# Kernel optimization log

Measured on AMD Instinct MI355X. Metric: run time of the kernel, lower is better.

Reference implementation:

```python
import jax, jax.numpy as jnp
import numpy as np

# dims: T time steps, B batch, CIN/COUT conv channels, HxW spatial, K kernel
T, B, CIN, COUT, H, Wd, K = 10, 32, 3, 64, 64, 64, 3
DECAY = 0.2      # LIF leak factor
INH = 1.625      # lateral inhibition strength (mode='threshold')


def setup_inputs() -> dict:
    key = jax.random.key(0)
    k1, k2 = jax.random.split(key)
    x = (jax.random.uniform(k1, (T, B, CIN, H, Wd)) < 0.2).astype(jnp.float32)
    W = jax.random.normal(k2, (COUT, CIN, K, K), dtype=jnp.float32)
    # normweight(): zero-mean, unit-std (biased) per output filter
    W = W - W.mean(axis=(1, 2, 3), keepdims=True)
    W = W / W.reshape(COUT, -1).std(axis=1).reshape(COUT, 1, 1, 1)
    return {"x": x, "W": W}


def _conv(x, W):
    # Conv2d stride=1, padding=1, no bias, NCHW/OIHW
    return jax.lax.conv_general_dilated(
        x, W, window_strides=(1, 1), padding=((1, 1), (1, 1)),
        dimension_numbers=("NCHW", "OIHW", "NCHW"))


def reference(x, W):
    def step(mem, x_t):
        i = _conv(x_t, W)                                        # (B,COUT,H,W)
        # ATB: adaptive per-channel threshold = max over batch+spatial
        thr = jnp.max(i, axis=(0, 2, 3), keepdims=True) + 1e-4   # (1,COUT,1,1)
        # ASF: clamp then thresholded sigmoid filter
        cur = jnp.maximum(i, 0.0)
        i_asf = thr * jax.nn.sigmoid((cur - 0.4 * thr) * (8.0 / thr))
        # LIF update with threshold = thr (set by ATB)
        mem = mem * DECAY + i_asf
        s = (mem > thr).astype(mem.dtype)                        # spikes 0/1
        # WTA k=1: keep only the strongest spiking channel per location
        score = mem * s
        winner = jnp.argmax(score, axis=1)                       # (B,H,W)
        oh = jnp.moveaxis(jax.nn.one_hot(winner, COUT, dtype=mem.dtype), -1, 1)
        s = s * oh
        # membrane reset of fired neurons
        mem = mem * (1.0 - s)
        # lateral inhibition: suppress non-winners at spiking locations
        any_sp = jnp.max(s, axis=1, keepdims=True)
        mem = mem - INH * thr * any_sp * (1.0 - s)
        return mem, s

    mem0 = jnp.zeros((B, COUT, H, Wd), jnp.float32)
    _, spikes = jax.lax.scan(step, mem0, x)
    return spikes  # (T,B,COUT,H,W)
```

## Files before the change

kernel.cpp:

```cpp
#include <hip/hip_runtime.h>
#include <math.h>

#define TT 10
#define BB 32
#define CIN 3
#define COUT 64
#define HH 64
#define WW 64
#define HW (HH*WW)
#define DECAY 0.2f
#define INH 1.625f

__device__ __forceinline__ unsigned int enc_f(float f) {
    unsigned int u = __float_as_uint(f);
    return (u & 0x80000000u) ? ~u : (u | 0x80000000u);
}
__device__ __forceinline__ float dec_f(unsigned int u) {
    u = (u & 0x80000000u) ? (u & 0x7FFFFFFFu) : ~u;
    return __uint_as_float(u);
}

__global__ __launch_bounds__(256) void thr_kernel(
    const float* __restrict__ x,
    const float* __restrict__ Wt,
    unsigned int* __restrict__ thr_raw,
    float* __restrict__ out)
{
    __shared__ float sx[CIN][6][68];
    __shared__ float wmax[4][COUT];

    const int tid  = threadIdx.x;
    const int lane = tid & 63;
    const int wave = tid >> 6;
    const int h0   = blockIdx.x * 4;
    const int b    = blockIdx.y;
    const int t    = blockIdx.z;

    float w[27];
    #pragma unroll
    for (int k = 0; k < 27; k++) w[k] = Wt[lane * 27 + k];

    const float* xb = x + ((size_t)t * BB + b) * (CIN * HW);
    for (int l = tid; l < CIN * 6 * 66; l += 256) {
        int ci  = l / 396;
        int r   = (l % 396) / 66;
        int col = l % 66;
        int gh = h0 + r - 1;
        int gw = col - 1;
        float v = 0.f;
        if (gh >= 0 && gh < HH && gw >= 0 && gw < WW)
            v = xb[ci * HW + gh * WW + gw];
        sx[ci][r][col] = v;
    }
    __syncthreads();

    float* ob = out + (((size_t)t * BB + b) * COUT) * HW;
    float mx = -INFINITY;

    for (int cc = 0; cc < 8; cc++) {
        #pragma unroll
        for (int k = 0; k < 2; k++) {
            int l   = (cc * 2 + k) * 256 + tid;
            int row = l >> 4;
            int q   = l & 15;
            int c   = row >> 2;
            int hr  = row & 3;
            *(float4*)(ob + (size_t)c * HW + (h0 + hr) * WW + q * 4) =
                make_float4(0.f, 0.f, 0.f, 0.f);
        }

        float acc[8];
        #pragma unroll
        for (int j = 0; j < 8; j++) acc[j] = 0.f;

        #pragma unroll
        for (int ci = 0; ci < CIN; ci++)
            #pragma unroll
            for (int kh = 0; kh < 3; kh++) {
                const float* rp = &sx[ci][wave + kh][cc * 8];
                float4 qa = *(const float4*)(rp + 0);
                float4 qb = *(const float4*)(rp + 4);
                float2 qc = *(const float2*)(rp + 8);
                float f0 = qa.x, f1 = qa.y, f2 = qa.z, f3 = qa.w;
                float f4 = qb.x, f5 = qb.y, f6 = qb.z, f7 = qb.w;
                float f8 = qc.x, f9 = qc.y;
                const float w0 = w[ci * 9 + kh * 3 + 0];
                const float w1 = w[ci * 9 + kh * 3 + 1];
                const float w2 = w[ci * 9 + kh * 3 + 2];
                acc[0] = fmaf(w0, f0, acc[0]); acc[0] = fmaf(w1, f1, acc[0]); acc[0] = fmaf(w2, f2, acc[0]);
                acc[1] = fmaf(w0, f1, acc[1]); acc[1] = fmaf(w1, f2, acc[1]); acc[1] = fmaf(w2, f3, acc[1]);
                acc[2] = fmaf(w0, f2, acc[2]); acc[2] = fmaf(w1, f3, acc[2]); acc[2] = fmaf(w2, f4, acc[2]);
                acc[3] = fmaf(w0, f3, acc[3]); acc[3] = fmaf(w1, f4, acc[3]); acc[3] = fmaf(w2, f5, acc[3]);
                acc[4] = fmaf(w0, f4, acc[4]); acc[4] = fmaf(w1, f5, acc[4]); acc[4] = fmaf(w2, f6, acc[4]);
                acc[5] = fmaf(w0, f5, acc[5]); acc[5] = fmaf(w1, f6, acc[5]); acc[5] = fmaf(w2, f7, acc[5]);
                acc[6] = fmaf(w0, f6, acc[6]); acc[6] = fmaf(w1, f7, acc[6]); acc[6] = fmaf(w2, f8, acc[6]);
                acc[7] = fmaf(w0, f7, acc[7]); acc[7] = fmaf(w1, f8, acc[7]); acc[7] = fmaf(w2, f9, acc[7]);
            }

        #pragma unroll
        for (int j = 0; j < 8; j++) mx = fmaxf(mx, acc[j]);
    }

    wmax[wave][lane] = mx;
    __syncthreads();
    if (wave == 0) {
        float m = fmaxf(fmaxf(wmax[0][lane], wmax[1][lane]),
                        fmaxf(wmax[2][lane], wmax[3][lane]));
        atomicMax(&thr_raw[t * COUT + lane], enc_f(m));
    }
}

__global__ __launch_bounds__(256) void fused_kernel(
    const float* __restrict__ x,
    const float* __restrict__ Wt,
    const unsigned int* __restrict__ thr_raw,
    float* __restrict__ out)
{
    __shared__ float sx[TT][CIN][3][36];

    const int tid  = threadIdx.x;
    const int lane = tid & 63;
    const int wave = tid >> 6;
    const int p0   = __builtin_amdgcn_readfirstlane(wave * 8);
    const int b    = blockIdx.x >> 7;
    const int h    = (blockIdx.x >> 1) & 63;
    const int w0   = (blockIdx.x & 1) << 5;

    float w[27];
    #pragma unroll
    for (int k = 0; k < 27; k++) w[k] = Wt[lane * 27 + k];

    {
        const float* xb0 = x + (size_t)b * (CIN * HW);
        for (int l = tid; l < TT * 306; l += 256) {
            int t   = l / 306;
            int r0  = l - t * 306;
            int ci  = r0 / 102;
            int r1  = r0 - ci * 102;
            int r   = r1 / 34;
            int col = r1 - r * 34;
            int gh = h + r - 1;
            int gw = w0 + col - 1;
            float v = 0.f;
            if (gh >= 0 && gh < HH && gw >= 0 && gw < WW)
                v = xb0[(size_t)t * ((size_t)BB * CIN * HW)
                        + ci * HW + gh * WW + gw];
            sx[t][ci][r][col] = v;
        }
    }

    float mem[8];
    #pragma unroll
    for (int j = 0; j < 8; j++) mem[j] = 0.f;

    __syncthreads();

    #pragma unroll 1
    for (int t = 0; t < TT; t++) {
        float thr   = dec_f(thr_raw[t * COUT + lane]) + 1e-4f;
        float sinv  = 8.0f / thr;
        float s04   = 0.4f * thr;
        float sinh_ = INH * thr;

        float acc[8];
        #pragma unroll
        for (int j = 0; j < 8; j++) acc[j] = 0.f;

        #pragma unroll
        for (int ci = 0; ci < CIN; ci++)
            #pragma unroll
            for (int kh = 0; kh < 3; kh++) {
                const float* rp = &sx[t][ci][kh][p0];
                float4 qa = *(const float4*)(rp + 0);
                float4 qb = *(const float4*)(rp + 4);
                float2 qc = *(const float2*)(rp + 8);
                float f0 = qa.x, f1 = qa.y, f2 = qa.z, f3 = qa.w;
                float f4 = qb.x, f5 = qb.y, f6 = qb.z, f7 = qb.w;
                float f8 = qc.x, f9 = qc.y;
                const float w0_ = w[ci * 9 + kh * 3 + 0];
                const float w1_ = w[ci * 9 + kh * 3 + 1];
                const float w2_ = w[ci * 9 + kh * 3 + 2];
                acc[0] = fmaf(w0_, f0, acc[0]); acc[0] = fmaf(w1_, f1, acc[0]); acc[0] = fmaf(w2_, f2, acc[0]);
                acc[1] = fmaf(w0_, f1, acc[1]); acc[1] = fmaf(w1_, f2, acc[1]); acc[1] = fmaf(w2_, f3, acc[1]);
                acc[2] = fmaf(w0_, f2, acc[2]); acc[2] = fmaf(w1_, f3, acc[2]); acc[2] = fmaf(w2_, f4, acc[2]);
                acc[3] = fmaf(w0_, f3, acc[3]); acc[3] = fmaf(w1_, f4, acc[3]); acc[3] = fmaf(w2_, f5, acc[3]);
                acc[4] = fmaf(w0_, f4, acc[4]); acc[4] = fmaf(w1_, f5, acc[4]); acc[4] = fmaf(w2_, f6, acc[4]);
                acc[5] = fmaf(w0_, f5, acc[5]); acc[5] = fmaf(w1_, f6, acc[5]); acc[5] = fmaf(w2_, f7, acc[5]);
                acc[6] = fmaf(w0_, f6, acc[6]); acc[6] = fmaf(w1_, f7, acc[6]); acc[6] = fmaf(w2_, f8, acc[6]);
                acc[7] = fmaf(w0_, f7, acc[7]); acc[7] = fmaf(w1_, f8, acc[7]); acc[7] = fmaf(w2_, f9, acc[7]);
            }

        int fmask = 0;

#define LIF_PX(J) {                                                         \
        float cur = fmaxf(acc[J], 0.f);                                     \
        float z   = (cur - s04) * sinv;                                     \
        float sig = 1.0f / (1.0f + expf(-z));                               \
        float m   = mem[J] * DECAY + thr * sig;                             \
        int   sp  = m > thr;                                                \
        float score = sp ? m : 0.f;                                         \
        unsigned long long blt = __ballot(sp);                              \
        int fr = 0, sp_any = 0;                                             \
        if (blt) {                                  \
            float bs = score;                                               \
            int   bc = lane;                                                \
            _Pragma("unroll")                                               \
            for (int off = 32; off > 0; off >>= 1) {                        \
                float so = __shfl_xor(bs, off, 64);                         \
                int   co = __shfl_xor(bc, off, 64);                         \
                if (so > bs || (so == bs && co < bc)) { bs = so; bc = co; } \
            }                                                               \
            int spw = __shfl(sp, bc, 64);      \
            fr     = (lane == bc) && sp;                                    \
            sp_any = spw;                                                   \
        }                                                                   \
        mem[J] = fr ? 0.f : (m - (sp_any ? sinh_ : 0.f));                   \
        if (fr) fmask |= (1 << (J));                                        \
    }

        LIF_PX(0); LIF_PX(1); LIF_PX(2); LIF_PX(3);
        LIF_PX(4); LIF_PX(5); LIF_PX(6); LIF_PX(7);
#undef LIF_PX

        if (fmask) {
            float* os = out + (((size_t)t * BB + b) * COUT) * HW + h * WW + w0;
            #pragma unroll
            for (int j = 0; j < 8; j++)
                if (fmask & (1 << j))
                    os[(size_t)lane * HW + p0 + j] = 1.0f;
        }
    }
}

extern "C" void kernel_launch(void* const* d_in, const int* in_sizes, int n_in,
                              void* d_out, int out_size, void* d_ws, size_t ws_size,
                              hipStream_t stream) {
    const float* x = (const float*)d_in[0];
    const float* W = (const float*)d_in[1];
    float* out     = (float*)d_out;

    unsigned int* thr = (unsigned int*)d_ws;
    hipMemsetAsync(thr, 0, TT * COUT * sizeof(unsigned int), stream);

    thr_kernel<<<dim3(HH / 4, BB, TT), 256, 0, stream>>>(x, W, thr, out);
    fused_kernel<<<dim3(BB * HH * 2), 256, 0, stream>>>(x, W, thr, out);
}
```

Before: 523.4 us.

## Pack two time steps into v_pk_fma_f32 for the 3x3 conv in both kernels

Shared-memory input tiles now hold pairs of time steps as float2. The convolution uses inline-asm v_pk_fma_f32 with op_sel to pick one weight and apply it to both time steps at once, which roughly halves the FMA instruction count in both the threshold and fused kernels. The threshold kernel grid is halved along time, with each block zeroing output for two steps. The fused kernel loops over 5 time pairs and runs the LIF/WTA logic twice per iteration. Costs are more register pressure from paired accumulators and the packed weight array, plus reliance on packed-FP32 support in the hardware.

```diff
diff --git a/kernel.cpp b/kernel.cpp
--- a/kernel.cpp
+++ b/kernel.cpp
@@ -11,6 +11,8 @@
 #define DECAY 0.2f
 #define INH 1.625f
 
+typedef __attribute__((ext_vector_type(2))) float f32x2;
+
 __device__ __forceinline__ unsigned int enc_f(float f) {
     unsigned int u = __float_as_uint(f);
     return (u & 0x80000000u) ? ~u : (u | 0x80000000u);
@@ -19,6 +21,42 @@
     u = (u & 0x80000000u) ? (u & 0x7FFFFFFFu) : ~u;
     return __uint_as_float(u);
 }
+
+__device__ __forceinline__ void pkfma_lo(f32x2& acc, f32x2 w2, f32x2 x2) {
+    asm("v_pk_fma_f32 %0, %1, %2, %0 op_sel:[0,0,0] op_sel_hi:[0,1,1]"
+        : "+v"(acc) : "v"(w2), "v"(x2));
+}
+__device__ __forceinline__ void pkfma_hi(f32x2& acc, f32x2 w2, f32x2 x2) {
+    asm("v_pk_fma_f32 %0, %1, %2, %0 op_sel:[1,0,0] op_sel_hi:[1,1,1]"
+        : "+v"(acc) : "v"(w2), "v"(x2));
+}
+#define CONV_TAP(ACC, FI, X2) { if ((FI) & 1) pkfma_hi(ACC, wp[(FI)>>1], X2); \
+                                else          pkfma_lo(ACC, wp[(FI)>>1], X2); }
+
+#define CKH(RP, FB)                                                           \
+    {                                                                         \
+        const f32x2* rp_ = (RP);                                              \
+        f32x2 d0 = rp_[0], d1 = rp_[1], d2 = rp_[2], d3 = rp_[3],             \
+              d4 = rp_[4], d5 = rp_[5], d6 = rp_[6], d7 = rp_[7],             \
+              d8 = rp_[8], d9 = rp_[9];                                       \
+        CONV_TAP(a0, (FB)+0, d0); CONV_TAP(a0, (FB)+1, d1); CONV_TAP(a0, (FB)+2, d2); \
+        CONV_TAP(a1, (FB)+0, d1); CONV_TAP(a1, (FB)+1, d2); CONV_TAP(a1, (FB)+2, d3); \
+        CONV_TAP(a2, (FB)+0, d2); CONV_TAP(a2, (FB)+1, d3); CONV_TAP(a2, (FB)+2, d4); \
+        CONV_TAP(a3, (FB)+0, d3); CONV_TAP(a3, (FB)+1, d4); CONV_TAP(a3, (FB)+2, d5); \
+        CONV_TAP(a4, (FB)+0, d4); CONV_TAP(a4, (FB)+1, d5); CONV_TAP(a4, (FB)+2, d6); \
+        CONV_TAP(a5, (FB)+0, d5); CONV_TAP(a5, (FB)+1, d6); CONV_TAP(a5, (FB)+2, d7); \
+        CONV_TAP(a6, (FB)+0, d6); CONV_TAP(a6, (FB)+1, d7); CONV_TAP(a6, (FB)+2, d8); \
+        CONV_TAP(a7, (FB)+0, d7); CONV_TAP(a7, (FB)+1, d8); CONV_TAP(a7, (FB)+2, d9); \
+    }
+
+#define LOAD_WP                                                               \
+    f32x2 wp[14];                                                             \
+    {                                                                         \
+        const float* wl = Wt + lane * 27;                                     \
+        _Pragma("unroll")                                                     \
+        for (int k = 0; k < 13; k++) { f32x2 t_; t_.x = wl[2*k]; t_.y = wl[2*k+1]; wp[k] = t_; } \
+        { f32x2 t_; t_.x = wl[26]; t_.y = wl[26]; wp[13] = t_; }              \
+    }
 
 __global__ __launch_bounds__(256) void thr_kernel(
     const float* __restrict__ x,
@@ -26,87 +64,73 @@
     unsigned int* __restrict__ thr_raw,
     float* __restrict__ out)
 {
-    __shared__ float sx[CIN][6][68];
-    __shared__ float wmax[4][COUT];
+    __shared__ f32x2 sx[CIN][6][68];
+    __shared__ float wmax[4][2][COUT];
 
     const int tid  = threadIdx.x;
     const int lane = tid & 63;
     const int wave = tid >> 6;
     const int h0   = blockIdx.x * 4;
     const int b    = blockIdx.y;
-    const int t    = blockIdx.z;
-
-    float w[27];
-    #pragma unroll
-    for (int k = 0; k < 27; k++) w[k] = Wt[lane * 27 + k];
-
-    const float* xb = x + ((size_t)t * BB + b) * (CIN * HW);
+    const int t0   = blockIdx.z * 2;
+
+    LOAD_WP
+
+    const float* xb0 = x + ((size_t)t0 * BB + b) * (CIN * HW);
+    const float* xb1 = xb0 + (size_t)BB * CIN * HW;
     for (int l = tid; l < CIN * 6 * 66; l += 256) {
         int ci  = l / 396;
         int r   = (l % 396) / 66;
         int col = l % 66;
         int gh = h0 + r - 1;
         int gw = col - 1;
-        float v = 0.f;
-        if (gh >= 0 && gh < HH && gw >= 0 && gw < WW)
-            v = xb[ci * HW + gh * WW + gw];
+        f32x2 v; v.x = 0.f; v.y = 0.f;
+        if (gh >= 0 && gh < HH && gw >= 0 && gw < WW) {
+            size_t off = (size_t)ci * HW + gh * WW + gw;
+            v.x = xb0[off];
+            v.y = xb1[off];
+        }
         sx[ci][r][col] = v;
     }
     __syncthreads();
 
-    float* ob = out + (((size_t)t * BB + b) * COUT) * HW;
-    float mx = -INFINITY;
+    float mx0 = -INFINITY, mx1 = -INFINITY;
 
     for (int cc = 0; cc < 8; cc++) {
         #pragma unroll
-        for (int k = 0; k < 2; k++) {
-            int l   = (cc * 2 + k) * 256 + tid;
-            int row = l >> 4;
+        for (int k = 0; k < 4; k++) {
+            int l   = cc * 1024 + k * 256 + tid;
+            int th  = l >> 12;
+            int row = (l >> 4) & 255;
             int q   = l & 15;
             int c   = row >> 2;
             int hr  = row & 3;
+            float* ob = out + (((size_t)(t0 + th) * BB + b) * COUT) * HW;
             *(float4*)(ob + (size_t)c * HW + (h0 + hr) * WW + q * 4) =
                 make_float4(0.f, 0.f, 0.f, 0.f);
         }
 
-        float acc[8];
-        #pragma unroll
-        for (int j = 0; j < 8; j++) acc[j] = 0.f;
-
+        f32x2 a0={0.f,0.f},a1={0.f,0.f},a2={0.f,0.f},a3={0.f,0.f},
+              a4={0.f,0.f},a5={0.f,0.f},a6={0.f,0.f},a7={0.f,0.f};
         #pragma unroll
         for (int ci = 0; ci < CIN; ci++)
             #pragma unroll
-            for (int kh = 0; kh < 3; kh++) {
-                const float* rp = &sx[ci][wave + kh][cc * 8];
-                float4 qa = *(const float4*)(rp + 0);
-                float4 qb = *(const float4*)(rp + 4);
-                float2 qc = *(const float2*)(rp + 8);
-                float f0 = qa.x, f1 = qa.y, f2 = qa.z, f3 = qa.w;
-                float f4 = qb.x, f5 = qb.y, f6 = qb.z, f7 = qb.w;
-                float f8 = qc.x, f9 = qc.y;
-                const float w0 = w[ci * 9 + kh * 3 + 0];
-                const float w1 = w[ci * 9 + kh * 3 + 1];
-                const float w2 = w[ci * 9 + kh * 3 + 2];
-                acc[0] = fmaf(w0, f0, acc[0]); acc[0] = fmaf(w1, f1, acc[0]); acc[0] = fmaf(w2, f2, acc[0]);
-                acc[1] = fmaf(w0, f1, acc[1]); acc[1] = fmaf(w1, f2, acc[1]); acc[1] = fmaf(w2, f3, acc[1]);
-                acc[2] = fmaf(w0, f2, acc[2]); acc[2] = fmaf(w1, f3, acc[2]); acc[2] = fmaf(w2, f4, acc[2]);
-                acc[3] = fmaf(w0, f3, acc[3]); acc[3] = fmaf(w1, f4, acc[3]); acc[3] = fmaf(w2, f5, acc[3]);
-                acc[4] = fmaf(w0, f4, acc[4]); acc[4] = fmaf(w1, f5, acc[4]); acc[4] = fmaf(w2, f6, acc[4]);
-                acc[5] = fmaf(w0, f5, acc[5]); acc[5] = fmaf(w1, f6, acc[5]); acc[5] = fmaf(w2, f7, acc[5]);
-                acc[6] = fmaf(w0, f6, acc[6]); acc[6] = fmaf(w1, f7, acc[6]); acc[6] = fmaf(w2, f8, acc[6]);
-                acc[7] = fmaf(w0, f7, acc[7]); acc[7] = fmaf(w1, f8, acc[7]); acc[7] = fmaf(w2, f9, acc[7]);
-            }
-
-        #pragma unroll
-        for (int j = 0; j < 8; j++) mx = fmaxf(mx, acc[j]);
-    }
-
-    wmax[wave][lane] = mx;
+            for (int kh = 0; kh < 3; kh++)
+                CKH(&sx[ci][wave + kh][cc * 8], ci * 9 + kh * 3);
+
+        mx0 = fmaxf(mx0, fmaxf(fmaxf(fmaxf(a0.x,a1.x),fmaxf(a2.x,a3.x)),
+                               fmaxf(fmaxf(a4.x,a5.x),fmaxf(a6.x,a7.x))));
+        mx1 = fmaxf(mx1, fmaxf(fmaxf(fmaxf(a0.y,a1.y),fmaxf(a2.y,a3.y)),
+                               fmaxf(fmaxf(a4.y,a5.y),fmaxf(a6.y,a7.y))));
+    }
+
+    wmax[wave][0][lane] = mx0;
+    wmax[wave][1][lane] = mx1;
     __syncthreads();
-    if (wave == 0) {
-        float m = fmaxf(fmaxf(wmax[0][lane], wmax[1][lane]),
-                        fmaxf(wmax[2][lane], wmax[3][lane]));
-        atomicMax(&thr_raw[t * COUT + lane], enc_f(m));
+    if (wave < 2) {
+        float m = fmaxf(fmaxf(wmax[0][wave][lane], wmax[1][wave][lane]),
+                        fmaxf(wmax[2][wave][lane], wmax[3][wave][lane]));
+        atomicMax(&thr_raw[(t0 + wave) * COUT + lane], enc_f(m));
     }
 }
 
@@ -116,7 +140,7 @@
     const unsigned int* __restrict__ thr_raw,
     float* __restrict__ out)
 {
-    __shared__ float sx[TT][CIN][3][36];
+    __shared__ f32x2 sx[5][CIN][3][36];
 
     const int tid  = threadIdx.x;
     const int lane = tid & 63;
@@ -126,26 +150,27 @@
     const int h    = (blockIdx.x >> 1) & 63;
     const int w0   = (blockIdx.x & 1) << 5;
 
-    float w[27];
-    #pragma unroll
-    for (int k = 0; k < 27; k++) w[k] = Wt[lane * 27 + k];
+    LOAD_WP
 
     {
         const float* xb0 = x + (size_t)b * (CIN * HW);
-        for (int l = tid; l < TT * 306; l += 256) {
-            int t   = l / 306;
-            int r0  = l - t * 306;
+        const size_t ts = (size_t)BB * CIN * HW;
+        for (int l = tid; l < 5 * 306; l += 256) {
+            int tp  = l / 306;
+            int r0  = l - tp * 306;
             int ci  = r0 / 102;
             int r1  = r0 - ci * 102;
             int r   = r1 / 34;
             int col = r1 - r * 34;
             int gh = h + r - 1;
             int gw = w0 + col - 1;
-            float v = 0.f;
-            if (gh >= 0 && gh < HH && gw >= 0 && gw < WW)
-                v = xb0[(size_t)t * ((size_t)BB * CIN * HW)
-                        + ci * HW + gh * WW + gw];
-            sx[t][ci][r][col] = v;
+            f32x2 v; v.x = 0.f; v.y = 0.f;
+            if (gh >= 0 && gh < HH && gw >= 0 && gw < WW) {
+                size_t off = (size_t)ci * HW + gh * WW + gw;
+                v.x = xb0[(size_t)(2 * tp)     * ts + off];
+                v.y = xb0[(size_t)(2 * tp + 1) * ts + off];
+            }
+            sx[tp][ci][r][col] = v;
         }
     }
 
@@ -155,45 +180,8 @@
 
     __syncthreads();
 
-    #pragma unroll 1
-    for (int t = 0; t < TT; t++) {
-        float thr   = dec_f(thr_raw[t * COUT + lane]) + 1e-4f;
-        float sinv  = 8.0f / thr;
-        float s04   = 0.4f * thr;
-        float sinh_ = INH * thr;
-
-        float acc[8];
-        #pragma unroll
-        for (int j = 0; j < 8; j++) acc[j] = 0.f;
-
-        #pragma unroll
-        for (int ci = 0; ci < CIN; ci++)
-            #pragma unroll
-            for (int kh = 0; kh < 3; kh++) {
-                const float* rp = &sx[t][ci][kh][p0];
-                float4 qa = *(const float4*)(rp + 0);
-                float4 qb = *(const float4*)(rp + 4);
-                float2 qc = *(const float2*)(rp + 8);
-                float f0 = qa.x, f1 = qa.y, f2 = qa.z, f3 = qa.w;
-                float f4 = qb.x, f5 = qb.y, f6 = qb.z, f7 = qb.w;
-                float f8 = qc.x, f9 = qc.y;
-                const float w0_ = w[ci * 9 + kh * 3 + 0];
-                const float w1_ = w[ci * 9 + kh * 3 + 1];
-                const float w2_ = w[ci * 9 + kh * 3 + 2];
-                acc[0] = fmaf(w0_, f0, acc[0]); acc[0] = fmaf(w1_, f1, acc[0]); acc[0] = fmaf(w2_, f2, acc[0]);
-                acc[1] = fmaf(w0_, f1, acc[1]); acc[1] = fmaf(w1_, f2, acc[1]); acc[1] = fmaf(w2_, f3, acc[1]);
-                acc[2] = fmaf(w0_, f2, acc[2]); acc[2] = fmaf(w1_, f3, acc[2]); acc[2] = fmaf(w2_, f4, acc[2]);
-                acc[3] = fmaf(w0_, f3, acc[3]); acc[3] = fmaf(w1_, f4, acc[3]); acc[3] = fmaf(w2_, f5, acc[3]);
-                acc[4] = fmaf(w0_, f4, acc[4]); acc[4] = fmaf(w1_, f5, acc[4]); acc[4] = fmaf(w2_, f6, acc[4]);
-                acc[5] = fmaf(w0_, f5, acc[5]); acc[5] = fmaf(w1_, f6, acc[5]); acc[5] = fmaf(w2_, f7, acc[5]);
-                acc[6] = fmaf(w0_, f6, acc[6]); acc[6] = fmaf(w1_, f7, acc[6]); acc[6] = fmaf(w2_, f8, acc[6]);
-                acc[7] = fmaf(w0_, f7, acc[7]); acc[7] = fmaf(w1_, f8, acc[7]); acc[7] = fmaf(w2_, f9, acc[7]);
-            }
-
-        int fmask = 0;
-
-#define LIF_PX(J) {                                                         \
-        float cur = fmaxf(acc[J], 0.f);                                     \
+#define LIF_PX(J, V) {                                                      \
+        float cur = fmaxf(V, 0.f);                                          \
         float z   = (cur - s04) * sinv;                                     \
         float sig = 1.0f / (1.0f + expf(-z));                               \
         float m   = mem[J] * DECAY + thr * sig;                             \
@@ -218,18 +206,55 @@
         if (fr) fmask |= (1 << (J));                                        \
     }
 
-        LIF_PX(0); LIF_PX(1); LIF_PX(2); LIF_PX(3);
-        LIF_PX(4); LIF_PX(5); LIF_PX(6); LIF_PX(7);
+    #pragma unroll 1
+    for (int tp = 0; tp < 5; tp++) {
+        unsigned int tru0 = thr_raw[(2 * tp)     * COUT + lane];
+        unsigned int tru1 = thr_raw[(2 * tp + 1) * COUT + lane];
+
+        f32x2 a0={0.f,0.f},a1={0.f,0.f},a2={0.f,0.f},a3={0.f,0.f},
+              a4={0.f,0.f},a5={0.f,0.f},a6={0.f,0.f},a7={0.f,0.f};
+        #pragma unroll
+        for (int ci = 0; ci < CIN; ci++)
+            #pragma unroll
+            for (int kh = 0; kh < 3; kh++)
+                CKH(&sx[tp][ci][kh][p0], ci * 9 + kh * 3);
+
+        {
+            float thr   = dec_f(tru0) + 1e-4f;
+            float sinv  = 8.0f / thr;
+            float s04   = 0.4f * thr;
+            float sinh_ = INH * thr;
+            int fmask = 0;
+            LIF_PX(0, a0.x); LIF_PX(1, a1.x); LIF_PX(2, a2.x); LIF_PX(3, a3.x);
+            LIF_PX(4, a4.x); LIF_PX(5, a5.x); LIF_PX(6, a6.x); LIF_PX(7, a7.x);
+            if (fmask) {
+                float* os = out + (((size_t)(2 * tp) * BB + b) * COUT) * HW
+                          + h * WW + w0;
+                #pragma unroll
+                for (int j = 0; j < 8; j++)
+                    if (fmask & (1 << j))
+                        os[(size_t)lane * HW + p0 + j] = 1.0f;
+            }
+        }
+        {
+            float thr   = dec_f(tru1) + 1e-4f;
+            float sinv  = 8.0f / thr;
+            float s04   = 0.4f * thr;
+            float sinh_ = INH * thr;
+            int fmask = 0;
+            LIF_PX(0, a0.y); LIF_PX(1, a1.y); LIF_PX(2, a2.y); LIF_PX(3, a3.y);
+            LIF_PX(4, a4.y); LIF_PX(5, a5.y); LIF_PX(6, a6.y); LIF_PX(7, a7.y);
+            if (fmask) {
+                float* os = out + (((size_t)(2 * tp + 1) * BB + b) * COUT) * HW
+                          + h * WW + w0;
+                #pragma unroll
+                for (int j = 0; j < 8; j++)
+                    if (fmask & (1 << j))
+                        os[(size_t)lane * HW + p0 + j] = 1.0f;
+            }
+        }
+    }
 #undef LIF_PX
-
-        if (fmask) {
-            float* os = out + (((size_t)t * BB + b) * COUT) * HW + h * WW + w0;
-            #pragma unroll
-            for (int j = 0; j < 8; j++)
-                if (fmask & (1 << j))
-                    os[(size_t)lane * HW + p0 + j] = 1.0f;
-        }
-    }
 }
 
 extern "C" void kernel_launch(void* const* d_in, const int* in_sizes, int n_in,
@@ -242,6 +267,6 @@
     unsigned int* thr = (unsigned int*)d_ws;
     hipMemsetAsync(thr, 0, TT * COUT * sizeof(unsigned int), stream);
 
-    thr_kernel<<<dim3(HH / 4, BB, TT), 256, 0, stream>>>(x, W, thr, out);
+    thr_kernel<<<dim3(HH / 4, BB, TT / 2), 256, 0, stream>>>(x, W, thr, out);
     fused_kernel<<<dim3(BB * HH * 2), 256, 0, stream>>>(x, W, thr, out);
 }
```

Result: faster. 494.1 us (-5.6%).
